# Kernel optimization log

Hardware: AMD Instinct MI355X
Metric: run time of the kernel (lower is better)

Reference implementation:

```python
import jax, jax.numpy as jnp
import numpy as np

HIDDEN = 4096
N_HEADS = 32
N_KV_HEADS = 8
HEAD_DIM = 128
EPS = 1e-6
ROPE_BASE = 1000000.0


def setup_inputs() -> dict:
    key = jax.random.key(0)
    ks = jax.random.split(key, 8)
    B, S = 4, 1024
    scale = 1.0 / np.sqrt(HIDDEN)
    return {
        "positions": jnp.arange(S, dtype=jnp.int32),
        "hidden_states": jax.random.normal(ks[0], (B, S, HIDDEN), jnp.float32),
        "wq": jax.random.normal(ks[1], (N_HEADS * HEAD_DIM, HIDDEN), jnp.float32) * scale,
        "wk": jax.random.normal(ks[2], (N_KV_HEADS * HEAD_DIM, HIDDEN), jnp.float32) * scale,
        "wv": jax.random.normal(ks[3], (N_KV_HEADS * HEAD_DIM, HIDDEN), jnp.float32) * scale,
        "wo": jax.random.normal(ks[4], (HIDDEN, N_HEADS * HEAD_DIM), jnp.float32) * scale,
        "q_norm_w": jnp.ones((HEAD_DIM,), jnp.float32),
        "k_norm_w": jnp.ones((HEAD_DIM,), jnp.float32),
    }


def _rms_norm(x, w):
    # normalize over last (head_dim) axis
    var = jnp.mean(jnp.square(x), axis=-1, keepdims=True)
    return x * jax.lax.rsqrt(var + EPS) * w


def _rope(x, positions):
    # neox-style rotary over full head_dim; x: [B, S, H, D]
    half = HEAD_DIM // 2
    inv_freq = 1.0 / (ROPE_BASE ** (jnp.arange(0, half, dtype=jnp.float32) * 2.0 / HEAD_DIM))
    ang = positions.astype(jnp.float32)[:, None] * inv_freq  # [S, half]
    cos = jnp.cos(ang)[None, :, None, :]
    sin = jnp.sin(ang)[None, :, None, :]
    x1, x2 = x[..., :half], x[..., half:]
    return jnp.concatenate([x1 * cos - x2 * sin, x2 * cos + x1 * sin], axis=-1)


def reference(positions, hidden_states, wq, wk, wv, wo, q_norm_w, k_norm_w):
    B, S, _ = hidden_states.shape
    q = jnp.einsum("bsd,qd->bsq", hidden_states, wq).reshape(B, S, N_HEADS, HEAD_DIM)
    k = jnp.einsum("bsd,kd->bsk", hidden_states, wk).reshape(B, S, N_KV_HEADS, HEAD_DIM)
    v = jnp.einsum("bsd,kd->bsk", hidden_states, wv).reshape(B, S, N_KV_HEADS, HEAD_DIM)
    q = _rms_norm(q, q_norm_w)
    k = _rms_norm(k, k_norm_w)
    q = _rope(q, positions)
    k = _rope(k, positions)
    # GQA: expand kv heads to query heads
    g = N_HEADS // N_KV_HEADS
    k = jnp.repeat(k, g, axis=2)  # [B, S, Hq, D]
    v = jnp.repeat(v, g, axis=2)
    scaling = HEAD_DIM ** -0.5
    scores = jnp.einsum("bqhd,bkhd->bhqk", q, k) * scaling
    probs = jax.nn.softmax(scores, axis=-1)  # ENCODER_ONLY: full bidirectional
    out = jnp.einsum("bhqk,bkhd->bqhd", probs, v).reshape(B, S, N_HEADS * HEAD_DIM)
    return jnp.einsum("bsq,dq->bsd", out, wo)
```

## Files before the change

kernel.cpp:

```cpp
#include <hip/hip_runtime.h>
#include <math.h>

#define SEQ    1024
#define BATCH  4
#define MROWS  4096
#define HID    4096
#define NHEADS 32
#define NKV    8
#define HDIM   128

typedef __bf16 bf16x8 __attribute__((ext_vector_type(8)));
typedef float  f32x4  __attribute__((ext_vector_type(4)));
typedef float  f32x16 __attribute__((ext_vector_type(16)));
typedef unsigned short u16x8 __attribute__((ext_vector_type(8)));
typedef unsigned short u16x4 __attribute__((ext_vector_type(4)));
typedef unsigned int   u32x4 __attribute__((ext_vector_type(4)));

static __device__ __forceinline__ unsigned short f2bf(float f) {
  union { float f; unsigned u; } x; x.f = f;
  unsigned r = x.u + 0x7fffu + ((x.u >> 16) & 1u);
  return (unsigned short)(r >> 16);
}
static __device__ __forceinline__ float bf2f(unsigned short h) {
  union { unsigned u; float f; } x; x.u = ((unsigned)h) << 16;
  return x.f;
}
static __device__ __forceinline__ unsigned cvtpk_bf16(float lo, float hi) {
  unsigned r;
  asm("v_cvt_pk_bf16_f32 %0, %1, %2" : "=v"(r) : "v"(lo), "v"(hi));
  return r;
}

static __device__ __forceinline__ void gload16(const unsigned short* g, unsigned short* l) {
  __builtin_amdgcn_global_load_lds(
      (const __attribute__((address_space(1))) unsigned int*)g,
      (__attribute__((address_space(3))) unsigned int*)l, 16, 0, 0);
}

__global__ __launch_bounds__(256) void cvt_kernel(const float* __restrict__ in,
                                                  unsigned short* __restrict__ out,
                                                  int n8) {
  int i = blockIdx.x * 256 + threadIdx.x;
  if (i >= n8) return;
  f32x4 a = ((const f32x4*)in)[2 * i];
  f32x4 b = ((const f32x4*)in)[2 * i + 1];
  u16x8 o;
  o[0] = f2bf(a[0]); o[1] = f2bf(a[1]); o[2] = f2bf(a[2]); o[3] = f2bf(a[3]);
  o[4] = f2bf(b[0]); o[5] = f2bf(b[1]); o[6] = f2bf(b[2]); o[7] = f2bf(b[3]);
  ((u16x8*)out)[i] = o;
}

template <int OUTMODE>
__global__ __launch_bounds__(256) void gemm_bt(const unsigned short* __restrict__ A,
                                               const unsigned short* __restrict__ B,
                                               void* __restrict__ Cp,
                                               int M, int N, int K, int ldc) {
  __shared__ unsigned short As[4096];
  __shared__ unsigned short Bs[4096];
  const int t  = threadIdx.x;
  const int l  = t & 63, w = t >> 6;
  const int wr = w >> 1, wc = w & 1;
  const int lr = l & 15, lg = l >> 4;
  const int m0 = blockIdx.y * 128, n0 = blockIdx.x * 128;

  const int srow = t >> 2;
  const int skg  = (t & 3) ^ (srow & 3);
  const unsigned short* ga0 = A + (long)(m0 + srow) * K + skg * 8;
  const unsigned short* ga1 = ga0 + 64L * K;
  const unsigned short* gb0 = B + (long)(n0 + srow) * K + skg * 8;
  const unsigned short* gb1 = gb0 + 64L * K;

  int aro[4], bro[4];
#pragma unroll
  for (int i = 0; i < 4; ++i) {
    aro[i] = (wr * 64 + i * 16 + lr) * 32 + ((lg ^ (lr & 3)) * 8);
    bro[i] = (wc * 64 + i * 16 + lr) * 32 + ((lg ^ (lr & 3)) * 8);
  }

  f32x4 acc[4][4] = {};
  for (int k0 = 0; k0 < K; k0 += 32) {
    if (k0) __syncthreads();
    gload16(ga0 + k0, As + (w << 9));
    gload16(ga1 + k0, As + 2048 + (w << 9));
    gload16(gb0 + k0, Bs + (w << 9));
    gload16(gb1 + k0, Bs + 2048 + (w << 9));
    __syncthreads();
    bf16x8 af[4], bfv[4];
#pragma unroll
    for (int i = 0; i < 4; ++i) af[i]  = *(const bf16x8*)(As + aro[i]);
#pragma unroll
    for (int i = 0; i < 4; ++i) bfv[i] = *(const bf16x8*)(Bs + bro[i]);
#pragma unroll
    for (int mi = 0; mi < 4; ++mi)
#pragma unroll
      for (int ni = 0; ni < 4; ++ni)
        acc[mi][ni] = __builtin_amdgcn_mfma_f32_16x16x32_bf16(af[mi], bfv[ni],
                                                              acc[mi][ni], 0, 0, 0);
  }

  const int r0 = m0 + wr * 64 + lg * 4;
  const int c0 = n0 + wc * 64 + lr;
  if (OUTMODE == 0) {
    unsigned short* C = (unsigned short*)Cp;
#pragma unroll
    for (int mi = 0; mi < 4; ++mi)
#pragma unroll
      for (int ni = 0; ni < 4; ++ni)
#pragma unroll
        for (int j = 0; j < 4; ++j)
          C[(long)(r0 + mi * 16 + j) * ldc + (c0 + ni * 16)] = f2bf(acc[mi][ni][j]);
  } else if (OUTMODE == 1) {
    float* C = (float*)Cp;
#pragma unroll
    for (int mi = 0; mi < 4; ++mi)
#pragma unroll
      for (int ni = 0; ni < 4; ++ni)
#pragma unroll
        for (int j = 0; j < 4; ++j)
          C[(long)(r0 + mi * 16 + j) * ldc + (c0 + ni * 16)] = acc[mi][ni][j];
  } else {
    unsigned short* C = (unsigned short*)Cp;
#pragma unroll
    for (int mi = 0; mi < 4; ++mi)
#pragma unroll
      for (int ni = 0; ni < 4; ++ni) {
        const int s_g   = r0 + mi * 16;
        const int d_g   = c0 + ni * 16;
        const int bb    = s_g >> 10;
        const int s_loc = s_g & 1023;
        const int kt_i  = s_loc >> 5;
        const int k_loc = s_loc & 31;
        const int kvh   = d_g >> 7;
        const int d_loc = d_g & 127;
        const int fxor  = (d_loc ^ (d_loc >> 2)) & 3;
        const long addr = ((long)((bb * NKV + kvh) * 32 + kt_i)) * 4096 +
                          d_loc * 32 + (((k_loc >> 3) ^ fxor) << 3) + (k_loc & 7);
        u16x4 v;
#pragma unroll
        for (int j = 0; j < 4; ++j) v[j] = f2bf(acc[mi][ni][j]);
        *(u16x4*)(C + addr) = v;
      }
  }
}

#define BAR8 __builtin_amdgcn_s_barrier()
#define WL0  do { asm volatile("s_waitcnt lgkmcnt(0)" ::: "memory"); \
                  __builtin_amdgcn_sched_barrier(0); } while (0)
#define WV6  asm volatile("s_waitcnt vmcnt(6)" ::: "memory")

template <int OUTMODE>
__global__ __launch_bounds__(512, 2) void gemm8_bt(const unsigned short* __restrict__ A,
                                                   const unsigned short* __restrict__ B,
                                                   void* __restrict__ Cp) {
  __shared__ unsigned short lds[65536];
  const int t = threadIdx.x, l = t & 63, w = t >> 6;
  const int wr = w >> 2, wc = w & 3;
  const int lr = l & 15, lg = l >> 4;
  const int bid = blockIdx.x;
  const int swz = (bid & 7) * 32 + (bid >> 3);
  const int m0 = (swz >> 4) << 8, n0 = (swz & 15) << 8;
  const long K = 4096;

  const int rc = l >> 3;
  const int ce = ((l & 7) ^ rc) << 3;

#define STGA(d, h, tt) do { \
    const unsigned short* _s = A + (long)(m0 + (h)*128 + w*8 + rc) * K + (long)(tt)*64 + ce; \
    gload16(_s,            lds + ((d)*2+(h))*8192 + w*512); \
    gload16(_s + 64L * K,  lds + ((d)*2+(h))*8192 + (8 + w)*512); \
  } while (0)
#define STGB(d, h, tt) do { \
    const unsigned short* _s = B + (long)(n0 + (h)*128 + w*8 + rc) * K + (long)(tt)*64 + ce; \
    gload16(_s,            lds + 32768 + ((d)*2+(h))*8192 + w*512); \
    gload16(_s + 64L * K,  lds + 32768 + ((d)*2+(h))*8192 + (8 + w)*512); \
  } while (0)
#define LDA8(d, rh) do { \
    _Pragma("unroll") for (int ri = 0; ri < 4; ++ri) \
    _Pragma("unroll") for (int kk = 0; kk < 2; ++kk) { \
      int r  = wr*64 + ri*16 + lr; \
      int cb = (kk*64 + lg*16) ^ ((l & 7) << 4); \
      a[ri][kk] = *(const bf16x8*)(lds + ((d)*2+(rh))*8192 + r*64 + (cb >> 1)); \
    } } while (0)
#define LDB8(d, ch, barr) do { \
    _Pragma("unroll") for (int ci = 0; ci < 2; ++ci) \
    _Pragma("unroll") for (int kk = 0; kk < 2; ++kk) { \
      int r  = wc*32 + ci*16 + lr; \
      int cb = (kk*64 + lg*16) ^ ((l & 7) << 4); \
      barr[ci][kk] = *(const bf16x8*)(lds + 32768 + ((d)*2+(ch))*8192 + r*64 + (cb >> 1)); \
    } } while (0)
#define MM8(rh, ch, barr) do { \
    __builtin_amdgcn_s_setprio(1); \
    _Pragma("unroll") for (int kk = 0; kk < 2; ++kk) \
    _Pragma("unroll") for (int ri = 0; ri < 4; ++ri) \
    _Pragma("unroll") for (int ci = 0; ci < 2; ++ci) \
      acc[rh][ch][ri][ci] = __builtin_amdgcn_mfma_f32_16x16x32_bf16( \
          a[ri][kk], barr[ci][kk], acc[rh][ch][ri][ci], 0, 0, 0); \
    __builtin_amdgcn_s_setprio(0); \
  } while (0)

  f32x4 acc[2][2][4][2] = {};
  bf16x8 a[4][2], b0[2][2], b1[2][2];

  STGA(0, 0, 0); STGB(0, 0, 0); STGB(0, 1, 0); STGA(0, 1, 0);
  STGA(1, 0, 1); STGB(1, 0, 1); STGB(1, 1, 1);
  WV6;
  BAR8;

  for (int i = 0; i < 32; ++i) {
    const int t1 = 2 * i + 1, t2 = (2 * i + 2) & 63, t3 = (2 * i + 3) & 63;
    LDA8(0, 0); LDB8(0, 0, b0);
    STGA(1, 1, t1);
    BAR8; WL0; MM8(0, 0, b0); BAR8;
    LDB8(0, 1, b1);
    STGA(0, 0, t2);
    BAR8; WL0; MM8(0, 1, b1); BAR8;
    LDA8(0, 1);
    STGB(0, 0, t2);
    BAR8; WL0; MM8(1, 1, b1); BAR8;
    STGB(0, 1, t2);
    WV6;
    BAR8; WL0; MM8(1, 0, b0); BAR8;
    LDA8(1, 0); LDB8(1, 0, b0);
    STGA(0, 1, t2);
    BAR8; WL0; MM8(0, 0, b0); BAR8;
    LDB8(1, 1, b1);
    STGA(1, 0, t3);
    BAR8; WL0; MM8(0, 1, b1); BAR8;
    LDA8(1, 1);
    STGB(1, 0, t3);
    BAR8; WL0; MM8(1, 1, b1); BAR8;
    STGB(1, 1, t3);
    WV6;
    BAR8; WL0; MM8(1, 0, b0); BAR8;
  }

#pragma unroll
  for (int rh = 0; rh < 2; ++rh)
#pragma unroll
    for (int ch = 0; ch < 2; ++ch)
#pragma unroll
      for (int ri = 0; ri < 4; ++ri)
#pragma unroll
        for (int ci = 0; ci < 2; ++ci)
#pragma unroll
          for (int j = 0; j < 4; ++j) {
            const int row = m0 + rh * 128 + wr * 64 + ri * 16 + lg * 4 + j;
            const int col = n0 + ch * 128 + wc * 32 + ci * 16 + lr;
            if (OUTMODE == 0)
              ((unsigned short*)Cp)[(long)row * 4096 + col] = f2bf(acc[rh][ch][ri][ci][j]);
            else
              ((float*)Cp)[(long)row * 4096 + col] = acc[rh][ch][ri][ci][j];
          }
#undef STGA
#undef STGB
#undef LDA8
#undef LDB8
#undef MM8
}

__global__ __launch_bounds__(256) void normrope_kernel(unsigned short* __restrict__ X,
                                                       const float* __restrict__ wnorm,
                                                       const int* __restrict__ positions,
                                                       int hshift, int stride) {
  const int t = threadIdx.x, l = t & 63, wv = t >> 6;
  const int slice = blockIdx.x * 4 + wv;
  const int head  = slice & ((1 << hshift) - 1);
  const int row   = slice >> hshift;
  const int s     = row & (SEQ - 1);
  unsigned short* p = X + (long)row * stride + (head << 7);

  float x1 = bf2f(p[l]), x2 = bf2f(p[l + 64]);
  float ss = x1 * x1 + x2 * x2;
#pragma unroll
  for (int m = 1; m < 64; m <<= 1) ss += __shfl_xor(ss, m, 64);
  float inv = rsqrtf(ss * (1.0f / 128.0f) + 1e-6f);
  x1 *= inv * wnorm[l];
  x2 *= inv * wnorm[l + 64];

  float invf = exp2f((float)l * -0.31143075889569023f);
  float ang  = (float)positions[s] * invf;
  float sn, cs;
  sincosf(ang, &sn, &cs);
  p[l]      = f2bf(x1 * cs - x2 * sn);
  p[l + 64] = f2bf(x2 * cs + x1 * sn);
}

__global__ __launch_bounds__(256, 3) void attn_kernel(const unsigned short* __restrict__ Q,
                                                      const unsigned short* __restrict__ Kb,
                                                      const unsigned short* __restrict__ Vtl,
                                                      unsigned short* __restrict__ O) {
  __shared__ unsigned short lds[24576];
  __shared__ float cl[4][32];
  const int t = threadIdx.x, l = t & 63, w = t >> 6;
  const int lq = l & 31, hi = l >> 5;
  const int blk = blockIdx.x;
  const int qb = blk & 7, h = (blk >> 3) & 31, b = blk >> 8;
  const int kv = h >> 2;
  const int q0 = qb * 128 + w * 32;

  const float qsc = 0.12751791438584222f;
  bf16x8 qf[8];
  const unsigned short* qrow = Q + (long)(b * SEQ + q0 + lq) * HID + h * HDIM + 8 * hi;
#pragma unroll
  for (int ks = 0; ks < 8; ++ks) {
    u16x8 raw = *(const u16x8*)(qrow + ks * 16);
    bf16x8 qv;
#pragma unroll
    for (int j = 0; j < 8; ++j) qv[j] = (__bf16)(bf2f(raw[j]) * qsc);
    qf[ks] = qv;
  }

  const unsigned short* Kg = Kb + (long)(b * SEQ) * 1024 + kv * HDIM;
  const unsigned short* Vg = Vtl + (long)(b * NKV + kv) * 32 * 4096;

#define STG_K(ring, ti) do { \
    _Pragma("unroll") for (int rr = 0; rr < 2; ++rr) { \
      int _row = (rr * 4 + w) * 4 + (l >> 4); \
      int _sc  = (l & 15) ^ (_row & 15); \
      gload16(Kg + (long)((ti) * 32 + _row) * 1024 + (_sc << 3), \
              lds + (ring) * 4096 + (rr * 4 + w) * 512); \
    } } while (0)
#define STG_V(ring, ti) do { \
    _Pragma("unroll") for (int rr = 0; rr < 2; ++rr) \
      gload16(Vg + (long)(ti) * 4096 + (((rr * 4 + w) * 64 + l) << 3), \
              lds + 12288 + (ring) * 4096 + (rr * 4 + w) * 512); \
    } while (0)

  f32x16 acc[4] = {};
  float m = -3.0e38f, lsum = 0.f;

  STG_K(0, 0); STG_V(0, 0);
  STG_K(1, 1); STG_V(1, 1);

  int ring = 0;
  for (int ti = 0; ti < 32; ++ti) {
    asm volatile("s_waitcnt vmcnt(4)" ::: "memory");
    __builtin_amdgcn_s_barrier();
    __builtin_amdgcn_sched_barrier(0);

    const int rstage = (ring >= 1) ? ring - 1 : 2;
    const int tn = (ti + 2) & 31;
    STG_K(rstage, tn); STG_V(rstage, tn);

    const unsigned short* kb = lds + ring * 4096 + lq * 128;
    bf16x8 kf[8];
#pragma unroll
    for (int ks = 0; ks < 8; ++ks)
      kf[ks] = *(const bf16x8*)(kb + ((((ks << 1) + hi) ^ (lq & 15)) << 3));
    f32x16 s = {};
    __builtin_amdgcn_s_setprio(1);
#pragma unroll
    for (int ks = 0; ks < 8; ++ks)
      s = __builtin_amdgcn_mfma_f32_32x32x16_bf16(kf[ks], qf[ks], s, 0, 0, 0);
    __builtin_amdgcn_s_setprio(0);

    float t0 = fmaxf(fmaxf(s[0], s[1]), fmaxf(s[2], s[3]));
    float t1 = fmaxf(fmaxf(s[4], s[5]), fmaxf(s[6], s[7]));
    float t2 = fmaxf(fmaxf(s[8], s[9]), fmaxf(s[10], s[11]));
    float t3 = fmaxf(fmaxf(s[12], s[13]), fmaxf(s[14], s[15]));
    float rm = fmaxf(fmaxf(t0, t1), fmaxf(t2, t3));
    rm = fmaxf(rm, __shfl_xor(rm, 32, 64));

    if (__any(rm > m + 8.0f)) {
      float mn = fmaxf(m, rm);
      float corr = exp2f(m - mn);
      m = mn;
      lsum *= corr;
      cl[w][lq] = corr;
      float cc[16];
#pragma unroll
      for (int r = 0; r < 16; ++r)
        cc[r] = cl[w][(r & 3) + 8 * (r >> 2) + 4 * hi];
#pragma unroll
      for (int db = 0; db < 4; ++db)
#pragma unroll
        for (int r = 0; r < 16; ++r) acc[db][r] *= cc[r];
    }

    float p[16];
    float ps = 0.f;
#pragma unroll
    for (int r = 0; r < 16; ++r) { p[r] = exp2f(s[r] - m); ps += p[r]; }
    lsum += ps + __shfl_xor(ps, 32, 64);

    bf16x8 pa[2];
#pragma unroll
    for (int c = 0; c < 2; ++c) {
      unsigned a0 = cvtpk_bf16(p[8 * c + 0], p[8 * c + 1]);
      unsigned b0 = cvtpk_bf16(p[8 * c + 4], p[8 * c + 5]);
      unsigned a1 = cvtpk_bf16(p[8 * c + 2], p[8 * c + 3]);
      unsigned b1 = cvtpk_bf16(p[8 * c + 6], p[8 * c + 7]);
      asm("v_permlane32_swap_b32 %0, %1" : "+v"(a0), "+v"(b0));
      asm("v_permlane32_swap_b32 %0, %1" : "+v"(a1), "+v"(b1));
      u32x4 w4 = {a0, a1, b0, b1};
      pa[c] = __builtin_bit_cast(bf16x8, w4);
    }

    __builtin_amdgcn_s_setprio(1);
#pragma unroll
    for (int db = 0; db < 4; ++db) {
      const int row = db * 32 + lq;
      const int fx  = (row ^ (row >> 2)) & 3;
      const unsigned short* vb = lds + 12288 + ring * 4096 + row * 32;
      bf16x8 v0 = *(const bf16x8*)(vb + ((hi ^ fx) << 3));
      bf16x8 v1 = *(const bf16x8*)(vb + (((2 + hi) ^ fx) << 3));
      acc[db] = __builtin_amdgcn_mfma_f32_32x32x16_bf16(pa[0], v0, acc[db], 0, 0, 0);
      acc[db] = __builtin_amdgcn_mfma_f32_32x32x16_bf16(pa[1], v1, acc[db], 0, 0, 0);
    }
    __builtin_amdgcn_s_setprio(0);

    ring = (ring < 2) ? ring + 1 : 0;
  }
#undef STG_K
#undef STG_V

  float il = 1.0f / lsum;
  cl[w][lq] = il;
  float ic[16];
#pragma unroll
  for (int r = 0; r < 16; ++r)
    ic[r] = cl[w][(r & 3) + 8 * (r >> 2) + 4 * hi];
#pragma unroll
  for (int db = 0; db < 4; ++db)
#pragma unroll
    for (int r = 0; r < 16; ++r) {
      int row = (r & 3) + 8 * (r >> 2) + 4 * hi;
      O[(long)(b * SEQ + q0 + row) * HID + h * HDIM + db * 32 + lq] =
          f2bf(acc[db][r] * ic[r]);
    }
}

extern "C" void kernel_launch(void* const* d_in, const int* in_sizes, int n_in,
                              void* d_out, int out_size, void* d_ws, size_t ws_size,
                              hipStream_t stream) {
  (void)in_sizes; (void)n_in; (void)out_size; (void)ws_size;
  const int*   positions = (const int*)d_in[0];
  const float* hs = (const float*)d_in[1];
  const float* wq = (const float*)d_in[2];
  const float* wk = (const float*)d_in[3];
  const float* wv = (const float*)d_in[4];
  const float* wo = (const float*)d_in[5];
  const float* qw = (const float*)d_in[6];
  const float* kw = (const float*)d_in[7];

  char* ws = (char*)d_ws;
  unsigned short* hs_b = (unsigned short*)(ws);
  unsigned short* wq_b = (unsigned short*)(ws + 33554432);
  unsigned short* wk_b = (unsigned short*)(ws + 67108864);
  unsigned short* wv_b = (unsigned short*)(ws + 75497472);
  unsigned short* wo_b = (unsigned short*)(ws + 83886080);
  unsigned short* q_b  = (unsigned short*)(ws + 117440512);
  unsigned short* k_b  = (unsigned short*)(ws + 150994944);
  unsigned short* vt_b = (unsigned short*)(ws + 159383552);
  unsigned short* ao_b = wq_b;

  cvt_kernel<<<dim3((16777216 / 8 + 255) / 256), dim3(256), 0, stream>>>(hs, hs_b, 16777216 / 8);
  cvt_kernel<<<dim3((16777216 / 8 + 255) / 256), dim3(256), 0, stream>>>(wq, wq_b, 16777216 / 8);
  cvt_kernel<<<dim3((4194304 / 8 + 255) / 256), dim3(256), 0, stream>>>(wk, wk_b, 4194304 / 8);
  cvt_kernel<<<dim3((4194304 / 8 + 255) / 256), dim3(256), 0, stream>>>(wv, wv_b, 4194304 / 8);
  cvt_kernel<<<dim3((16777216 / 8 + 255) / 256), dim3(256), 0, stream>>>(wo, wo_b, 16777216 / 8);

  gemm8_bt<0><<<dim3(256), dim3(512), 0, stream>>>(hs_b, wq_b, q_b);
  gemm_bt<0><<<dim3(8, 32), dim3(256), 0, stream>>>(hs_b, wk_b, k_b, 4096, 1024, 4096, 1024);
  gemm_bt<3><<<dim3(8, 32), dim3(256), 0, stream>>>(hs_b, wv_b, vt_b, 4096, 1024, 4096, 0);

  normrope_kernel<<<dim3(32768), dim3(256), 0, stream>>>(q_b, qw, positions, 5, 4096);
  normrope_kernel<<<dim3(8192), dim3(256), 0, stream>>>(k_b, kw, positions, 3, 1024);

  attn_kernel<<<dim3(1024), dim3(256), 0, stream>>>(q_b, k_b, vt_b, ao_b);

  gemm8_bt<1><<<dim3(256), dim3(512), 0, stream>>>(ao_b, wo_b, (float*)d_out);
}
```

Baseline: 588.0 us.

## Software-pipeline QK^T one tile ahead in attention and merge conversion kernels

The attention loop now computes the next tile's QK^T MFMAs before running softmax and PV on the current tile, so matrix work overlaps the exp/max math. To support this, the LDS ring grows from three to four stages (64KB total) and occupancy drops from three to two blocks per CU. Separately, the five fp32-to-bf16 conversion launches are merged into one kernel that picks its source by block index, which saves launch gaps. The deeper pipeline costs LDS and occupancy, and the extra live accumulators raise register pressure.

```diff
diff --git a/kernel.cpp b/kernel.cpp
--- a/kernel.cpp
+++ b/kernel.cpp
@@ -37,11 +37,24 @@
       (__attribute__((address_space(3))) unsigned int*)l, 16, 0, 0);
 }
 
-__global__ __launch_bounds__(256) void cvt_kernel(const float* __restrict__ in,
-                                                  unsigned short* __restrict__ out,
-                                                  int n8) {
-  int i = blockIdx.x * 256 + threadIdx.x;
-  if (i >= n8) return;
+__global__ __launch_bounds__(256) void cvt_all(const float* __restrict__ hs,
+                                               const float* __restrict__ wq,
+                                               const float* __restrict__ wk,
+                                               const float* __restrict__ wv,
+                                               const float* __restrict__ wo,
+                                               unsigned short* __restrict__ hs_b,
+                                               unsigned short* __restrict__ wq_b,
+                                               unsigned short* __restrict__ wk_b,
+                                               unsigned short* __restrict__ wv_b,
+                                               unsigned short* __restrict__ wo_b) {
+  const int bid = blockIdx.x;
+  const float* in; unsigned short* out; int base;
+  if (bid < 8192)       { in = hs; out = hs_b; base = 0; }
+  else if (bid < 16384) { in = wq; out = wq_b; base = 8192; }
+  else if (bid < 18432) { in = wk; out = wk_b; base = 16384; }
+  else if (bid < 20480) { in = wv; out = wv_b; base = 18432; }
+  else                  { in = wo; out = wo_b; base = 20480; }
+  const int i = (bid - base) * 256 + threadIdx.x;
   f32x4 a = ((const f32x4*)in)[2 * i];
   f32x4 b = ((const f32x4*)in)[2 * i + 1];
   u16x8 o;
@@ -285,11 +298,11 @@
   p[l + 64] = f2bf(x2 * cs + x1 * sn);
 }
 
-__global__ __launch_bounds__(256, 3) void attn_kernel(const unsigned short* __restrict__ Q,
+__global__ __launch_bounds__(256, 2) void attn_kernel(const unsigned short* __restrict__ Q,
                                                       const unsigned short* __restrict__ Kb,
                                                       const unsigned short* __restrict__ Vtl,
                                                       unsigned short* __restrict__ O) {
-  __shared__ unsigned short lds[24576];
+  __shared__ unsigned short lds[32768];
   __shared__ float cl[4][32];
   const int t = threadIdx.x, l = t & 63, w = t >> 6;
   const int lq = l & 31, hi = l >> 5;
@@ -323,41 +336,48 @@
 #define STG_V(ring, ti) do { \
     _Pragma("unroll") for (int rr = 0; rr < 2; ++rr) \
       gload16(Vg + (long)(ti) * 4096 + (((rr * 4 + w) * 64 + l) << 3), \
-              lds + 12288 + (ring) * 4096 + (rr * 4 + w) * 512); \
+              lds + 16384 + (ring) * 4096 + (rr * 4 + w) * 512); \
     } while (0)
+#define QKT(dst, ring) do { \
+    const unsigned short* kb = lds + (ring) * 4096 + lq * 128; \
+    bf16x8 kf[8]; \
+    _Pragma("unroll") for (int ks = 0; ks < 8; ++ks) \
+      kf[ks] = *(const bf16x8*)(kb + ((((ks << 1) + hi) ^ (lq & 15)) << 3)); \
+    __builtin_amdgcn_s_setprio(1); \
+    _Pragma("unroll") for (int ks = 0; ks < 8; ++ks) \
+      dst = __builtin_amdgcn_mfma_f32_32x32x16_bf16(kf[ks], qf[ks], dst, 0, 0, 0); \
+    __builtin_amdgcn_s_setprio(0); \
+  } while (0)
 
   f32x16 acc[4] = {};
   float m = -3.0e38f, lsum = 0.f;
 
   STG_K(0, 0); STG_V(0, 0);
   STG_K(1, 1); STG_V(1, 1);
-
-  int ring = 0;
+  STG_K(2, 2); STG_V(2, 2);
+  asm volatile("s_waitcnt vmcnt(8)" ::: "memory");
+  __builtin_amdgcn_s_barrier();
+  __builtin_amdgcn_sched_barrier(0);
+
+  f32x16 s_cur = {};
+  QKT(s_cur, 0);
+
+#pragma unroll 2
   for (int ti = 0; ti < 32; ++ti) {
     asm volatile("s_waitcnt vmcnt(4)" ::: "memory");
     __builtin_amdgcn_s_barrier();
     __builtin_amdgcn_sched_barrier(0);
 
-    const int rstage = (ring >= 1) ? ring - 1 : 2;
-    const int tn = (ti + 2) & 31;
-    STG_K(rstage, tn); STG_V(rstage, tn);
-
-    const unsigned short* kb = lds + ring * 4096 + lq * 128;
-    bf16x8 kf[8];
-#pragma unroll
-    for (int ks = 0; ks < 8; ++ks)
-      kf[ks] = *(const bf16x8*)(kb + ((((ks << 1) + hi) ^ (lq & 15)) << 3));
-    f32x16 s = {};
-    __builtin_amdgcn_s_setprio(1);
-#pragma unroll
-    for (int ks = 0; ks < 8; ++ks)
-      s = __builtin_amdgcn_mfma_f32_32x32x16_bf16(kf[ks], qf[ks], s, 0, 0, 0);
-    __builtin_amdgcn_s_setprio(0);
-
-    float t0 = fmaxf(fmaxf(s[0], s[1]), fmaxf(s[2], s[3]));
-    float t1 = fmaxf(fmaxf(s[4], s[5]), fmaxf(s[6], s[7]));
-    float t2 = fmaxf(fmaxf(s[8], s[9]), fmaxf(s[10], s[11]));
-    float t3 = fmaxf(fmaxf(s[12], s[13]), fmaxf(s[14], s[15]));
+    const int rs = (ti + 3) & 3, tn = (ti + 3) & 31;
+    STG_K(rs, tn); STG_V(rs, tn);
+
+    f32x16 s_next = {};
+    QKT(s_next, (ti + 1) & 3);
+
+    float t0 = fmaxf(fmaxf(s_cur[0], s_cur[1]), fmaxf(s_cur[2], s_cur[3]));
+    float t1 = fmaxf(fmaxf(s_cur[4], s_cur[5]), fmaxf(s_cur[6], s_cur[7]));
+    float t2 = fmaxf(fmaxf(s_cur[8], s_cur[9]), fmaxf(s_cur[10], s_cur[11]));
+    float t3 = fmaxf(fmaxf(s_cur[12], s_cur[13]), fmaxf(s_cur[14], s_cur[15]));
     float rm = fmaxf(fmaxf(t0, t1), fmaxf(t2, t3));
     rm = fmaxf(rm, __shfl_xor(rm, 32, 64));
 
@@ -380,7 +400,7 @@
     float p[16];
     float ps = 0.f;
 #pragma unroll
-    for (int r = 0; r < 16; ++r) { p[r] = exp2f(s[r] - m); ps += p[r]; }
+    for (int r = 0; r < 16; ++r) { p[r] = exp2f(s_cur[r] - m); ps += p[r]; }
     lsum += ps + __shfl_xor(ps, 32, 64);
 
     bf16x8 pa[2];
@@ -401,7 +421,7 @@
     for (int db = 0; db < 4; ++db) {
       const int row = db * 32 + lq;
       const int fx  = (row ^ (row >> 2)) & 3;
-      const unsigned short* vb = lds + 12288 + ring * 4096 + row * 32;
+      const unsigned short* vb = lds + 16384 + (ti & 3) * 4096 + row * 32;
       bf16x8 v0 = *(const bf16x8*)(vb + ((hi ^ fx) << 3));
       bf16x8 v1 = *(const bf16x8*)(vb + (((2 + hi) ^ fx) << 3));
       acc[db] = __builtin_amdgcn_mfma_f32_32x32x16_bf16(pa[0], v0, acc[db], 0, 0, 0);
@@ -409,10 +429,11 @@
     }
     __builtin_amdgcn_s_setprio(0);
 
-    ring = (ring < 2) ? ring + 1 : 0;
+    s_cur = s_next;
   }
 #undef STG_K
 #undef STG_V
+#undef QKT
 
   float il = 1.0f / lsum;
   cl[w][lq] = il;
@@ -454,11 +475,8 @@
   unsigned short* vt_b = (unsigned short*)(ws + 159383552);
   unsigned short* ao_b = wq_b;
 
-  cvt_kernel<<<dim3((16777216 / 8 + 255) / 256), dim3(256), 0, stream>>>(hs, hs_b, 16777216 / 8);
-  cvt_kernel<<<dim3((16777216 / 8 + 255) / 256), dim3(256), 0, stream>>>(wq, wq_b, 16777216 / 8);
-  cvt_kernel<<<dim3((4194304 / 8 + 255) / 256), dim3(256), 0, stream>>>(wk, wk_b, 4194304 / 8);
-  cvt_kernel<<<dim3((4194304 / 8 + 255) / 256), dim3(256), 0, stream>>>(wv, wv_b, 4194304 / 8);
-  cvt_kernel<<<dim3((16777216 / 8 + 255) / 256), dim3(256), 0, stream>>>(wo, wo_b, 16777216 / 8);
+  cvt_all<<<dim3(28672), dim3(256), 0, stream>>>(hs, wq, wk, wv, wo,
+                                                 hs_b, wq_b, wk_b, wv_b, wo_b);
 
   gemm8_bt<0><<<dim3(256), dim3(512), 0, stream>>>(hs_b, wq_b, q_b);
   gemm_bt<0><<<dim3(8, 32), dim3(256), 0, stream>>>(hs_b, wk_b, k_b, 4096, 1024, 4096, 1024);
```

After: 568.8 us. -3.3%, faster.
